# Kernel tuning notes

Measured on AMD Instinct MI355X. Metric: run time of the kernel, lower is better.

The kernel has to match this reference:

```python
import jax, jax.numpy as jnp
import numpy as np

H = 4  # num_heads

def setup_inputs() -> dict:
    key = jax.random.key(0)
    ks = jax.random.split(key, 9)
    B, S, D = 8, 2048, 256
    x = jax.random.normal(ks[0], (B, S, D), dtype=jnp.float32)
    scale = 1.0 / np.sqrt(D)
    Wq = jax.random.normal(ks[1], (D, D), dtype=jnp.float32) * scale
    bq = jnp.zeros((D,), dtype=jnp.float32)
    Wk = jax.random.normal(ks[2], (D, D), dtype=jnp.float32) * scale
    bk = jnp.zeros((D,), dtype=jnp.float32)
    Wv = jax.random.normal(ks[3], (D, D), dtype=jnp.float32) * scale
    bv = jnp.zeros((D,), dtype=jnp.float32)
    Wo = jax.random.normal(ks[4], (D, D), dtype=jnp.float32) * scale
    bo = jnp.zeros((D,), dtype=jnp.float32)
    return {"x": x, "Wq": Wq, "bq": bq, "Wk": Wk, "bk": bk,
            "Wv": Wv, "bv": bv, "Wo": Wo, "bo": bo}

def reference(x, Wq, bq, Wk, bk, Wv, bv, Wo, bo):
    B, S, D = x.shape
    hd = D // H
    inv_scale = 1.0 / jnp.sqrt(jnp.asarray(hd, x.dtype))
    # projections: torch Linear is x @ W.T + b; weights here stored as (D, D) used as x @ W + b
    def split_heads(t):
        return t.reshape(B, S, H, hd).transpose(0, 2, 1, 3)  # [B,H,S,hd]
    Q = split_heads(x @ Wq + bq)
    K = split_heads(x @ Wk + bk)
    V = split_heads(x @ Wv + bv)
    scores = jnp.einsum('bhqd,bhkd->bhqk', Q, K) * inv_scale  # [B,H,S,S]
    attn = jax.nn.softmax(scores, axis=-1)
    # dropout is identity in eval mode
    ctx = jnp.einsum('bhqk,bhkd->bhqd', attn, V)
    ctx = ctx.transpose(0, 2, 1, 3).reshape(B, S, D)
    return ctx @ Wo + bo
```

## Files before the change

kernel.cpp:

```cpp
#include <hip/hip_runtime.h>


typedef unsigned short u16;
typedef __bf16 bf16x8 __attribute__((ext_vector_type(8)));
typedef float  f32x4  __attribute__((ext_vector_type(4)));
typedef unsigned int u32x4 __attribute__((ext_vector_type(4)));
typedef unsigned int u32x2 __attribute__((ext_vector_type(2)));

#define LOG2E   1.4426950408889634f
#define ATTN_SC (0.125f * LOG2E)
#define PSTR    2097152
#define WPSTR   32768
#define WZSTR   65536

__device__ __forceinline__ u16 f2b(float f) {
  unsigned u = __builtin_bit_cast(unsigned, f);
  u += 0x7FFFu + ((u >> 16) & 1u);
  return (u16)(u >> 16);
}
__device__ __forceinline__ float b2f(u16 b) {
  return __builtin_bit_cast(float, (unsigned)b << 16);
}
__device__ __forceinline__ unsigned pack_trunc(float a, float b) {
  return (__builtin_bit_cast(unsigned, a) >> 16) | (__builtin_bit_cast(unsigned, b) & 0xFFFF0000u);
}
__device__ __forceinline__ unsigned pack_rne(float a, float b) {
  return (unsigned)f2b(a) | ((unsigned)f2b(b) << 16);
}
__device__ __forceinline__ f32x4 mfma16(bf16x8 a, bf16x8 b, f32x4 c) {
  return __builtin_amdgcn_mfma_f32_16x16x32_bf16(a, b, c, 0, 0, 0);
}
__device__ __forceinline__ void cp16(const u16* g, u16* l) {
  __builtin_amdgcn_global_load_lds((const __attribute__((address_space(1))) void*)g,
                                   (__attribute__((address_space(3))) void*)l, 16, 0, 0);
}

template <typename T>
__global__ __launch_bounds__(256) void prep(const T* __restrict__ x,
                                            const T* __restrict__ W0, const T* __restrict__ W1,
                                            const T* __restrict__ W2, const T* __restrict__ W3,
                                            const T* __restrict__ b0, const T* __restrict__ b1,
                                            const T* __restrict__ b2, const T* __restrict__ b3,
                                            u16* __restrict__ xp, u16* __restrict__ WTp,
                                            float* __restrict__ biasf) {
  int bid = blockIdx.x;
  if (bid < 4096) {
    int i0 = (bid * 256 + threadIdx.x) * 4;
    int row = i0 >> 8, col = i0 & 255;
    int p = col >> 7, pc = col & 127;
    u16* o = xp + (size_t)p * PSTR + (size_t)row * 128 + pc;
#pragma unroll
    for (int j = 0; j < 4; ++j) {
      if constexpr (sizeof(T) == 4) o[j] = f2b((float)x[i0 + j]);
      else                          o[j] = (u16)x[i0 + j];
    }
  } else {
    bid -= 4096;
    const int z = bid >> 8;
    const T* W = z == 0 ? W0 : z == 1 ? W1 : z == 2 ? W2 : W3;
    const T* b = z == 0 ? b0 : z == 1 ? b1 : z == 2 ? b2 : b3;
    int idx = (bid & 255) * 256 + threadIdx.x;
    int k = idx >> 8, n = idx & 255;
    u16 wb;
    if constexpr (sizeof(T) == 4) wb = f2b((float)W[k * 256 + n]);
    else                          wb = (u16)W[k * 256 + n];
    WTp[z * WZSTR + (k >> 7) * WPSTR + n * 128 + (k & 127)] = wb;
    if (idx < 256) {
      float bv;
      if constexpr (sizeof(T) == 4) bv = (float)b[idx];
      else                          bv = b2f((u16)b[idx]);
      biasf[z * 256 + idx] = bv;
    }
  }
}

__global__ __launch_bounds__(256, 2) void qkv_gemm(const u16* __restrict__ xp, const u16* __restrict__ WTp,
                                                   const float* __restrict__ biasf,
                                                   u16* __restrict__ Qw, u16* __restrict__ Kw,
                                                   u16* __restrict__ VTg) {
  __shared__ __align__(16) u16 Al[128 * 128];
  __shared__ __align__(16) u16 Bl[3][64 * 128];
  const int tid = threadIdx.x, w = tid >> 6, lane = tid & 63;
  const int l16 = lane & 15, quad = lane >> 4;
  const int n0 = blockIdx.y * 64, m0 = blockIdx.x * 128;
  f32x4 acc[3][2][4];
#pragma unroll
  for (int z = 0; z < 3; ++z)
#pragma unroll
    for (int mm = 0; mm < 2; ++mm)
#pragma unroll
      for (int nb = 0; nb < 4; ++nb) acc[z][mm][nb] = (f32x4){0.f, 0.f, 0.f, 0.f};

#pragma unroll
  for (int p = 0; p < 2; ++p) {
    __syncthreads();
    const u16* Ap = xp + (size_t)m0 * 128 + (size_t)p * PSTR;
#pragma unroll
    for (int i = 0; i < 8; ++i) {
      int slot = i * 256 + w * 64 + lane;
      int row = slot >> 4, pc = slot & 15, c = pc ^ (row & 15);
      cp16(Ap + (size_t)row * 128 + c * 8, Al + (i * 256 + w * 64) * 8);
    }
#pragma unroll
    for (int z = 0; z < 3; ++z) {
      const u16* Bp = WTp + z * WZSTR + n0 * 128 + p * WPSTR;
#pragma unroll
      for (int i = 0; i < 4; ++i) {
        int slot = i * 256 + w * 64 + lane;
        int row = slot >> 4, pc = slot & 15, c = pc ^ (row & 15);
        cp16(Bp + (size_t)row * 128 + c * 8, Bl[z] + (i * 256 + w * 64) * 8);
      }
    }
    __syncthreads();
#pragma unroll
    for (int kc = 0; kc < 4; ++kc) {
      bf16x8 a0 = *(const bf16x8*)&Al[(w * 32 + l16) * 128 + (((kc * 4 + quad) ^ l16)) * 8];
      bf16x8 a1 = *(const bf16x8*)&Al[(w * 32 + 16 + l16) * 128 + (((kc * 4 + quad) ^ l16)) * 8];
#pragma unroll
      for (int z = 0; z < 3; ++z)
#pragma unroll
        for (int nb = 0; nb < 4; ++nb) {
          bf16x8 b = *(const bf16x8*)&Bl[z][(nb * 16 + l16) * 128 + (((kc * 4 + quad) ^ l16)) * 8];
          acc[z][0][nb] = mfma16(a0, b, acc[z][0][nb]);
          acc[z][1][nb] = mfma16(a1, b, acc[z][1][nb]);
        }
    }
  }

  const int bb = m0 >> 11, s0 = m0 & 2047, h = blockIdx.y;
#pragma unroll
  for (int z = 0; z < 2; ++z) {
    u16* dst = (z == 0) ? Qw : Kw;
    const float sc = (z == 0) ? ATTN_SC : 1.0f;
    const float* bp = biasf + z * 256;
#pragma unroll
    for (int mm = 0; mm < 2; ++mm)
#pragma unroll
      for (int nb = 0; nb < 4; ++nb) {
        int d = nb * 16 + l16;
        float bv = bp[n0 + d];
#pragma unroll
        for (int r = 0; r < 4; ++r) {
          int s = s0 + w * 32 + mm * 16 + quad * 4 + r;
          dst[(((size_t)(bb * 4 + h) * 2048) + s) * 64 + d] = f2b((acc[z][mm][nb][r] + bv) * sc);
        }
      }
  }
  __syncthreads();
  {
    const float* bp = biasf + 2 * 256;
#pragma unroll
    for (int mm = 0; mm < 2; ++mm)
#pragma unroll
      for (int nb = 0; nb < 4; ++nb) {
        int d = nb * 16 + l16;
        float bv = bp[n0 + d];
        f32x4 v = acc[2][mm][nb];
        u32x2 dd = { pack_rne(v[0] + bv, v[1] + bv), pack_rne(v[2] + bv, v[3] + bv) };
        int cch = w * 4 + mm * 2 + (quad >> 1);
        *(u32x2*)&Bl[0][d * 128 + ((cch ^ (d & 15))) * 8 + (quad & 1) * 4] = dd;
      }
    __syncthreads();
#pragma unroll
    for (int i = 0; i < 4; ++i) {
      int slot = i * 256 + tid;
      int d = slot >> 4, pc = slot & 15;
      u32x4 vv = *(const u32x4*)&Bl[0][d * 128 + ((pc ^ (d & 15))) * 8];
      *(u32x4*)(VTg + (((size_t)(bb * 4 + h) * 64) + d) * 2048 + s0 + pc * 8) = vv;
    }
  }
}

template <bool OUT_BF16>
__global__ __launch_bounds__(256, 2) void out_gemm(const u16* __restrict__ ctxp, const u16* __restrict__ WTp,
                                                   const float* __restrict__ bo, void* __restrict__ outv) {
  __shared__ __align__(16) u16 Al[128 * 128];
  __shared__ __align__(16) u16 Bl[128 * 128];
  const int tid = threadIdx.x, w = tid >> 6, lane = tid & 63;
  const int l16 = lane & 15, quad = lane >> 4;
  const int n0 = blockIdx.y * 128, m0 = blockIdx.x * 128;
  f32x4 acc[2][8];
#pragma unroll
  for (int mm = 0; mm < 2; ++mm)
#pragma unroll
    for (int nb = 0; nb < 8; ++nb) acc[mm][nb] = (f32x4){0.f, 0.f, 0.f, 0.f};

#pragma unroll
  for (int p = 0; p < 2; ++p) {
    __syncthreads();
    const u16* Ap = ctxp + (size_t)m0 * 128 + (size_t)p * PSTR;
    const u16* Bp = WTp + 3 * WZSTR + n0 * 128 + p * WPSTR;
#pragma unroll
    for (int i = 0; i < 8; ++i) {
      int slot = i * 256 + w * 64 + lane;
      int row = slot >> 4, pc = slot & 15, c = pc ^ (row & 15);
      cp16(Ap + (size_t)row * 128 + c * 8, Al + (i * 256 + w * 64) * 8);
    }
#pragma unroll
    for (int i = 0; i < 8; ++i) {
      int slot = i * 256 + w * 64 + lane;
      int row = slot >> 4, pc = slot & 15, c = pc ^ (row & 15);
      cp16(Bp + (size_t)row * 128 + c * 8, Bl + (i * 256 + w * 64) * 8);
    }
    __syncthreads();
#pragma unroll
    for (int kc = 0; kc < 4; ++kc) {
      bf16x8 a0 = *(const bf16x8*)&Al[(w * 32 + l16) * 128 + (((kc * 4 + quad) ^ l16)) * 8];
      bf16x8 a1 = *(const bf16x8*)&Al[(w * 32 + 16 + l16) * 128 + (((kc * 4 + quad) ^ l16)) * 8];
#pragma unroll
      for (int nb = 0; nb < 8; ++nb) {
        bf16x8 b = *(const bf16x8*)&Bl[(nb * 16 + l16) * 128 + (((kc * 4 + quad) ^ l16)) * 8];
        acc[0][nb] = mfma16(a0, b, acc[0][nb]);
        acc[1][nb] = mfma16(a1, b, acc[1][nb]);
      }
    }
  }

#pragma unroll
  for (int mm = 0; mm < 2; ++mm)
#pragma unroll
    for (int nb = 0; nb < 8; ++nb) {
      int n = n0 + nb * 16 + l16;
      float bv = bo[n];
#pragma unroll
      for (int r = 0; r < 4; ++r) {
        size_t m = m0 + w * 32 + mm * 16 + quad * 4 + r;
        float v = acc[mm][nb][r] + bv;
        if constexpr (OUT_BF16) ((u16*)outv)[m * 256 + n] = f2b(v);
        else                    ((float*)outv)[m * 256 + n] = v;
      }
    }
}

__global__ __launch_bounds__(256, 2) void attn(const u16* __restrict__ Q, const u16* __restrict__ K,
                                               const u16* __restrict__ VT, u16* __restrict__ ctxp) {
  __shared__ __align__(16) u16 Kt[2][64 * 64];
  __shared__ __align__(16) u16 VTt[2][64 * 64];
  __shared__ __align__(16) u16 Pt[4][16 * 64];
  const int tid = threadIdx.x;
  const int w = tid >> 6, lane = tid & 63;
  const int l16 = lane & 15, quad = lane >> 4;
  const int bh = blockIdx.y, q0 = blockIdx.x * 128;
  const u16* Qp = Q + (size_t)bh * 2048 * 64;
  const u16* Kp = K + (size_t)bh * 2048 * 64;
  const u16* Vp = VT + (size_t)bh * 64 * 2048;
  u16* Ptw = Pt[w];

  bf16x8 qf[2][2];
#pragma unroll
  for (int h = 0; h < 2; ++h) {
    int qrow = q0 + w * 32 + h * 16 + l16;
    qf[h][0] = *(const bf16x8*)(Qp + (size_t)qrow * 64 + quad * 8);
    qf[h][1] = *(const bf16x8*)(Qp + (size_t)qrow * 64 + 32 + quad * 8);
  }

  f32x4 acc[2][4];
#pragma unroll
  for (int h = 0; h < 2; ++h)
#pragma unroll
    for (int nb = 0; nb < 4; ++nb) acc[h][nb] = (f32x4){0.f, 0.f, 0.f, 0.f};
  float dn0 = 0.f, dn1 = 0.f;

  const int sl0 = w * 64 + lane, sl1 = 256 + w * 64 + lane;
  const int r0 = sl0 >> 3, c0 = (sl0 & 7) ^ (r0 & 7);
  const int r1 = sl1 >> 3, c1 = (sl1 & 7) ^ (r1 & 7);
  const int pr0 = (r0 & 0x20) | ((r0 & 0x0C) << 1) | ((r0 & 0x10) >> 2) | (r0 & 3);
  const int pr1 = (r1 & 0x20) | ((r1 & 0x0C) << 1) | ((r1 & 0x10) >> 2) | (r1 & 3);

#define STAGE(kt_, buf_)                                                               \
  do {                                                                                 \
    cp16(Kp + (size_t)((kt_) * 64 + pr0) * 64 + c0 * 8, &Kt[buf_][(w * 64) * 8]);      \
    cp16(Kp + (size_t)((kt_) * 64 + pr1) * 64 + c1 * 8, &Kt[buf_][(256 + w * 64) * 8]);\
    cp16(Vp + (size_t)r0 * 2048 + (kt_) * 64 + c0 * 8, &VTt[buf_][(w * 64) * 8]);      \
    cp16(Vp + (size_t)r1 * 2048 + (kt_) * 64 + c1 * 8, &VTt[buf_][(256 + w * 64) * 8]);\
  } while (0)

  STAGE(0, 0);

  for (int kt = 0; kt < 32; ++kt) {
    const int buf = kt & 1;
    __builtin_amdgcn_s_waitcnt(0x0F70 );
    __asm__ __volatile__("" ::: "memory");
    __builtin_amdgcn_s_barrier();
    __asm__ __volatile__("" ::: "memory");
    if (kt < 31) STAGE(kt + 1, buf ^ 1);

    const u16* KtB = Kt[buf];
    const u16* VtB = VTt[buf];

    bf16x8 kfr[2][4];
#pragma unroll
    for (int kc = 0; kc < 2; ++kc)
#pragma unroll
      for (int nbK = 0; nbK < 4; ++nbK)
        kfr[kc][nbK] = *(const bf16x8*)&KtB[(nbK * 16 + l16) * 64 + (((kc * 4 + quad) ^ (l16 & 7))) * 8];
    bf16x8 vbr[2][4];
#pragma unroll
    for (int m = 0; m < 2; ++m)
#pragma unroll
      for (int nbD = 0; nbD < 4; ++nbD)
        vbr[m][nbD] = *(const bf16x8*)&VtB[(nbD * 16 + l16) * 64 + (((m * 4 + quad) ^ (l16 & 7))) * 8];

#pragma unroll
    for (int h = 0; h < 2; ++h) {
      f32x4 st[4];
#pragma unroll
      for (int nb = 0; nb < 4; ++nb) st[nb] = (f32x4){0.f, 0.f, 0.f, 0.f};
#pragma unroll
      for (int kc = 0; kc < 2; ++kc)
#pragma unroll
        for (int nbK = 0; nbK < 4; ++nbK)
          st[nbK] = mfma16(kfr[kc][nbK], qf[h][kc], st[nbK]);

      unsigned pw[8];
      float d = 0.f;
#pragma unroll
      for (int nbK = 0; nbK < 4; ++nbK) {
        float p0 = __builtin_amdgcn_exp2f(st[nbK][0]);
        float p1 = __builtin_amdgcn_exp2f(st[nbK][1]);
        float p2 = __builtin_amdgcn_exp2f(st[nbK][2]);
        float p3 = __builtin_amdgcn_exp2f(st[nbK][3]);
        d += (p0 + p1) + (p2 + p3);
        pw[nbK * 2]     = pack_trunc(p0, p1);
        pw[nbK * 2 + 1] = pack_trunc(p2, p3);
      }
      if (h == 0) dn0 += d; else dn1 += d;
      bf16x8 pb0 = __builtin_bit_cast(bf16x8, (u32x4){pw[0], pw[1], pw[2], pw[3]});
      bf16x8 pb1 = __builtin_bit_cast(bf16x8, (u32x4){pw[4], pw[5], pw[6], pw[7]});

#pragma unroll
      for (int nbD = 0; nbD < 4; ++nbD) acc[h][nbD] = mfma16(vbr[0][nbD], pb0, acc[h][nbD]);
#pragma unroll
      for (int nbD = 0; nbD < 4; ++nbD) acc[h][nbD] = mfma16(vbr[1][nbD], pb1, acc[h][nbD]);
    }
  }
#undef STAGE

  float linv0, linv1;
  { float d = dn0; d += __shfl_xor(d, 16); d += __shfl_xor(d, 32); linv0 = 1.0f / d; }
  { float d = dn1; d += __shfl_xor(d, 16); d += __shfl_xor(d, 32); linv1 = 1.0f / d; }

  const int bb = bh >> 2, hh = bh & 3;
  const int p = hh >> 1, pcol = (hh & 1) * 64;
#pragma unroll
  for (int h = 0; h < 2; ++h) {
    const float linv = h ? linv1 : linv0;
#pragma unroll
    for (int nbD = 0; nbD < 4; ++nbD) {
      f32x4 v = acc[h][nbD];
      u32x2 dd = { pack_rne(v[0] * linv, v[1] * linv), pack_rne(v[2] * linv, v[3] * linv) };
      int cch = nbD * 2 + (quad >> 1);
      *(u32x2*)&Ptw[l16 * 64 + ((cch ^ (l16 & 7))) * 8 + (quad & 1) * 4] = dd;
    }
    __asm__ __volatile__("" ::: "memory");
#pragma unroll
    for (int cc2 = 0; cc2 < 2; ++cc2) {
      int slot = cc2 * 64 + lane;
      int row = slot >> 3, pc = slot & 7;
      u32x4 vv = *(const u32x4*)&Ptw[row * 64 + ((pc ^ (row & 7))) * 8];
      size_t m = (size_t)bb * 2048 + q0 + w * 32 + h * 16 + row;
      *(u32x4*)&ctxp[(size_t)p * PSTR + m * 128 + pcol + pc * 8] = vv;
    }
    __asm__ __volatile__("" ::: "memory");
  }
}

extern "C" void kernel_launch(void* const* d_in, const int* in_sizes, int n_in,
                              void* d_out, int out_size, void* d_ws, size_t ws_size,
                              hipStream_t stream) {
  bool f32in = true;
  {
    void* basep = nullptr; size_t sz = 0;
    hipError_t e = hipMemGetAddressRange((hipDeviceptr_t*)&basep, &sz, (hipDeviceptr_t)d_in[0]);
    if (e == hipSuccess && sz > 0) f32in = sz >= (size_t)in_sizes[0] * 4;
    else f32in = false;
  }

  char* ws = (char*)d_ws;
  u16*   xp    = (u16*)(ws + 0);
  u16*   ctxp  = xp;
  u16*   WTp   = (u16*)(ws + 8388608);
  float* biasf = (float*)(ws + 8912896);
  u16*   Qw    = (u16*)(ws + 8916992);
  u16*   Kw    = (u16*)(ws + 17305600);
  u16*   VTg   = (u16*)(ws + 25694208);

  dim3 blk(256);
  if (f32in) {
    prep<float><<<5120, blk, 0, stream>>>(
        (const float*)d_in[0],
        (const float*)d_in[1], (const float*)d_in[3], (const float*)d_in[5], (const float*)d_in[7],
        (const float*)d_in[2], (const float*)d_in[4], (const float*)d_in[6], (const float*)d_in[8],
        xp, WTp, biasf);
  } else {
    prep<u16><<<5120, blk, 0, stream>>>(
        (const u16*)d_in[0],
        (const u16*)d_in[1], (const u16*)d_in[3], (const u16*)d_in[5], (const u16*)d_in[7],
        (const u16*)d_in[2], (const u16*)d_in[4], (const u16*)d_in[6], (const u16*)d_in[8],
        xp, WTp, biasf);
  }
  qkv_gemm<<<dim3(128, 4), blk, 0, stream>>>(xp, WTp, biasf, Qw, Kw, VTg);
  attn<<<dim3(16, 32), blk, 0, stream>>>(Qw, Kw, VTg, ctxp);
  if (f32in) out_gemm<false><<<dim3(128, 2), blk, 0, stream>>>(ctxp, WTp, biasf + 3 * 256, d_out);
  else       out_gemm<true ><<<dim3(128, 2), blk, 0, stream>>>(ctxp, WTp, biasf + 3 * 256, d_out);
}
```

Measured before the change: 146.2 us.

## Use two waves per attention block with 64 query rows each

The attention kernel now launches 128 threads per block instead of 256, and each wave handles 64 query rows instead of 32. Each K/V fragment loaded from shared memory is therefore reused across four 16-row query groups, which halves LDS read traffic per FLOP. The K and V fragment registers share one array so register pressure stays manageable. The cost is fewer waves per block and more accumulator registers per wave, which may lower occupancy and latency hiding, and each thread now issues twice as many global-to-LDS copies per stage.

```diff
diff --git a/kernel.cpp b/kernel.cpp
--- a/kernel.cpp
+++ b/kernel.cpp
@@ -232,11 +232,11 @@
     }
 }
 
-__global__ __launch_bounds__(256, 2) void attn(const u16* __restrict__ Q, const u16* __restrict__ K,
+__global__ __launch_bounds__(128, 1) void attn(const u16* __restrict__ Q, const u16* __restrict__ K,
                                                const u16* __restrict__ VT, u16* __restrict__ ctxp) {
   __shared__ __align__(16) u16 Kt[2][64 * 64];
   __shared__ __align__(16) u16 VTt[2][64 * 64];
-  __shared__ __align__(16) u16 Pt[4][16 * 64];
+  __shared__ __align__(16) u16 Pt[2][16 * 64];
   const int tid = threadIdx.x;
   const int w = tid >> 6, lane = tid & 63;
   const int l16 = lane & 15, quad = lane >> 4;
@@ -246,33 +246,40 @@
   const u16* Vp = VT + (size_t)bh * 64 * 2048;
   u16* Ptw = Pt[w];
 
-  bf16x8 qf[2][2];
-#pragma unroll
-  for (int h = 0; h < 2; ++h) {
-    int qrow = q0 + w * 32 + h * 16 + l16;
+  bf16x8 qf[4][2];
+#pragma unroll
+  for (int h = 0; h < 4; ++h) {
+    int qrow = q0 + w * 64 + h * 16 + l16;
     qf[h][0] = *(const bf16x8*)(Qp + (size_t)qrow * 64 + quad * 8);
     qf[h][1] = *(const bf16x8*)(Qp + (size_t)qrow * 64 + 32 + quad * 8);
   }
 
-  f32x4 acc[2][4];
-#pragma unroll
-  for (int h = 0; h < 2; ++h)
+  f32x4 acc[4][4];
+#pragma unroll
+  for (int h = 0; h < 4; ++h)
 #pragma unroll
     for (int nb = 0; nb < 4; ++nb) acc[h][nb] = (f32x4){0.f, 0.f, 0.f, 0.f};
-  float dn0 = 0.f, dn1 = 0.f;
-
-  const int sl0 = w * 64 + lane, sl1 = 256 + w * 64 + lane;
-  const int r0 = sl0 >> 3, c0 = (sl0 & 7) ^ (r0 & 7);
-  const int r1 = sl1 >> 3, c1 = (sl1 & 7) ^ (r1 & 7);
-  const int pr0 = (r0 & 0x20) | ((r0 & 0x0C) << 1) | ((r0 & 0x10) >> 2) | (r0 & 3);
-  const int pr1 = (r1 & 0x20) | ((r1 & 0x0C) << 1) | ((r1 & 0x10) >> 2) | (r1 & 3);
-
-#define STAGE(kt_, buf_)                                                               \
-  do {                                                                                 \
-    cp16(Kp + (size_t)((kt_) * 64 + pr0) * 64 + c0 * 8, &Kt[buf_][(w * 64) * 8]);      \
-    cp16(Kp + (size_t)((kt_) * 64 + pr1) * 64 + c1 * 8, &Kt[buf_][(256 + w * 64) * 8]);\
-    cp16(Vp + (size_t)r0 * 2048 + (kt_) * 64 + c0 * 8, &VTt[buf_][(w * 64) * 8]);      \
-    cp16(Vp + (size_t)r1 * 2048 + (kt_) * 64 + c1 * 8, &VTt[buf_][(256 + w * 64) * 8]);\
+  float dn[4] = {0.f, 0.f, 0.f, 0.f};
+
+  int rr[4], cc[4], pr[4];
+#pragma unroll
+  for (int i = 0; i < 4; ++i) {
+    int sl = i * 128 + w * 64 + lane;
+    rr[i] = sl >> 3;
+    cc[i] = (sl & 7) ^ (rr[i] & 7);
+    pr[i] = (rr[i] & 0x20) | ((rr[i] & 0x0C) << 1) | ((rr[i] & 0x10) >> 2) | (rr[i] & 3);
+  }
+
+#define STAGE(kt_, buf_)                                                                   \
+  do {                                                                                     \
+    _Pragma("unroll")                                                                      \
+    for (int i = 0; i < 4; ++i)                                                            \
+      cp16(Kp + (size_t)((kt_) * 64 + pr[i]) * 64 + cc[i] * 8,                             \
+           &Kt[buf_][(i * 128 + w * 64) * 8]);                                             \
+    _Pragma("unroll")                                                                      \
+    for (int i = 0; i < 4; ++i)                                                            \
+      cp16(Vp + (size_t)rr[i] * 2048 + (kt_) * 64 + cc[i] * 8,                             \
+           &VTt[buf_][(i * 128 + w * 64) * 8]);                                            \
   } while (0)
 
   STAGE(0, 0);
@@ -288,21 +295,16 @@
     const u16* KtB = Kt[buf];
     const u16* VtB = VTt[buf];
 
-    bf16x8 kfr[2][4];
+    bf16x8 fr[2][4];
 #pragma unroll
     for (int kc = 0; kc < 2; ++kc)
 #pragma unroll
       for (int nbK = 0; nbK < 4; ++nbK)
-        kfr[kc][nbK] = *(const bf16x8*)&KtB[(nbK * 16 + l16) * 64 + (((kc * 4 + quad) ^ (l16 & 7))) * 8];
-    bf16x8 vbr[2][4];
-#pragma unroll
-    for (int m = 0; m < 2; ++m)
-#pragma unroll
-      for (int nbD = 0; nbD < 4; ++nbD)
-        vbr[m][nbD] = *(const bf16x8*)&VtB[(nbD * 16 + l16) * 64 + (((m * 4 + quad) ^ (l16 & 7))) * 8];
-
-#pragma unroll
-    for (int h = 0; h < 2; ++h) {
+        fr[kc][nbK] = *(const bf16x8*)&KtB[(nbK * 16 + l16) * 64 + (((kc * 4 + quad) ^ (l16 & 7))) * 8];
+
+    bf16x8 pb[4][2];
+#pragma unroll
+    for (int h = 0; h < 4; ++h) {
       f32x4 st[4];
 #pragma unroll
       for (int nb = 0; nb < 4; ++nb) st[nb] = (f32x4){0.f, 0.f, 0.f, 0.f};
@@ -310,7 +312,7 @@
       for (int kc = 0; kc < 2; ++kc)
 #pragma unroll
         for (int nbK = 0; nbK < 4; ++nbK)
-          st[nbK] = mfma16(kfr[kc][nbK], qf[h][kc], st[nbK]);
+          st[nbK] = mfma16(fr[kc][nbK], qf[h][kc], st[nbK]);
 
       unsigned pw[8];
       float d = 0.f;
@@ -324,31 +326,45 @@
         pw[nbK * 2]     = pack_trunc(p0, p1);
         pw[nbK * 2 + 1] = pack_trunc(p2, p3);
       }
-      if (h == 0) dn0 += d; else dn1 += d;
-      bf16x8 pb0 = __builtin_bit_cast(bf16x8, (u32x4){pw[0], pw[1], pw[2], pw[3]});
-      bf16x8 pb1 = __builtin_bit_cast(bf16x8, (u32x4){pw[4], pw[5], pw[6], pw[7]});
-
-#pragma unroll
-      for (int nbD = 0; nbD < 4; ++nbD) acc[h][nbD] = mfma16(vbr[0][nbD], pb0, acc[h][nbD]);
-#pragma unroll
-      for (int nbD = 0; nbD < 4; ++nbD) acc[h][nbD] = mfma16(vbr[1][nbD], pb1, acc[h][nbD]);
+      dn[h] += d;
+      pb[h][0] = __builtin_bit_cast(bf16x8, (u32x4){pw[0], pw[1], pw[2], pw[3]});
+      pb[h][1] = __builtin_bit_cast(bf16x8, (u32x4){pw[4], pw[5], pw[6], pw[7]});
+    }
+
+#pragma unroll
+    for (int m = 0; m < 2; ++m)
+#pragma unroll
+      for (int nbD = 0; nbD < 4; ++nbD)
+        fr[m][nbD] = *(const bf16x8*)&VtB[(nbD * 16 + l16) * 64 + (((m * 4 + quad) ^ (l16 & 7))) * 8];
+
+#pragma unroll
+    for (int h = 0; h < 4; ++h) {
+#pragma unroll
+      for (int nbD = 0; nbD < 4; ++nbD) acc[h][nbD] = mfma16(fr[0][nbD], pb[h][0], acc[h][nbD]);
+#pragma unroll
+      for (int nbD = 0; nbD < 4; ++nbD) acc[h][nbD] = mfma16(fr[1][nbD], pb[h][1], acc[h][nbD]);
     }
   }
 #undef STAGE
 
-  float linv0, linv1;
-  { float d = dn0; d += __shfl_xor(d, 16); d += __shfl_xor(d, 32); linv0 = 1.0f / d; }
-  { float d = dn1; d += __shfl_xor(d, 16); d += __shfl_xor(d, 32); linv1 = 1.0f / d; }
+  float linv[4];
+#pragma unroll
+  for (int h = 0; h < 4; ++h) {
+    float d = dn[h];
+    d += __shfl_xor(d, 16);
+    d += __shfl_xor(d, 32);
+    linv[h] = 1.0f / d;
+  }
 
   const int bb = bh >> 2, hh = bh & 3;
   const int p = hh >> 1, pcol = (hh & 1) * 64;
 #pragma unroll
-  for (int h = 0; h < 2; ++h) {
-    const float linv = h ? linv1 : linv0;
+  for (int h = 0; h < 4; ++h) {
 #pragma unroll
     for (int nbD = 0; nbD < 4; ++nbD) {
       f32x4 v = acc[h][nbD];
-      u32x2 dd = { pack_rne(v[0] * linv, v[1] * linv), pack_rne(v[2] * linv, v[3] * linv) };
+      u32x2 dd = { pack_rne(v[0] * linv[h], v[1] * linv[h]),
+                   pack_rne(v[2] * linv[h], v[3] * linv[h]) };
       int cch = nbD * 2 + (quad >> 1);
       *(u32x2*)&Ptw[l16 * 64 + ((cch ^ (l16 & 7))) * 8 + (quad & 1) * 4] = dd;
     }
@@ -358,7 +374,7 @@
       int slot = cc2 * 64 + lane;
       int row = slot >> 3, pc = slot & 7;
       u32x4 vv = *(const u32x4*)&Ptw[row * 64 + ((pc ^ (row & 7))) * 8];
-      size_t m = (size_t)bb * 2048 + q0 + w * 32 + h * 16 + row;
+      size_t m = (size_t)bb * 2048 + q0 + w * 64 + h * 16 + row;
       *(u32x4*)&ctxp[(size_t)p * PSTR + m * 128 + pcol + pc * 8] = vv;
     }
     __asm__ __volatile__("" ::: "memory");
@@ -400,7 +416,7 @@
         xp, WTp, biasf);
   }
   qkv_gemm<<<dim3(128, 4), blk, 0, stream>>>(xp, WTp, biasf, Qw, Kw, VTg);
-  attn<<<dim3(16, 32), blk, 0, stream>>>(Qw, Kw, VTg, ctxp);
+  attn<<<dim3(16, 32), dim3(128), 0, stream>>>(Qw, Kw, VTg, ctxp);
   if (f32in) out_gemm<false><<<dim3(128, 2), blk, 0, stream>>>(ctxp, WTp, biasf + 3 * 256, d_out);
   else       out_gemm<true ><<<dim3(128, 2), blk, 0, stream>>>(ctxp, WTp, biasf + 3 * 256, d_out);
 }
```

New measurement: 164.3 us. +12.4%, slower.

## Triple-buffer K/V tiles in attention and raise wave priority around MFMAs

Applied to the files above, without the earlier changes.

The attention loop moves from double to triple buffering of the K and V^T LDS tiles, prefetching two tiles ahead. The waitcnt is relaxed so the oldest tile can complete while the next one is still in flight. s_setprio is raised around the MFMA blocks so waves issuing matrix ops get scheduling preference. LDS use grows from 32KB to 48KB for K/V, which may limit occupancy against the launch bound of two blocks per CU. Rotating the buffer pointers at run time may also add address arithmetic.

```diff
diff --git a/kernel.cpp b/kernel.cpp
--- a/kernel.cpp
+++ b/kernel.cpp
@@ -234,8 +234,8 @@
 
 __global__ __launch_bounds__(256, 2) void attn(const u16* __restrict__ Q, const u16* __restrict__ K,
                                                const u16* __restrict__ VT, u16* __restrict__ ctxp) {
-  __shared__ __align__(16) u16 Kt[2][64 * 64];
-  __shared__ __align__(16) u16 VTt[2][64 * 64];
+  __shared__ __align__(16) u16 Kt[3][64 * 64];
+  __shared__ __align__(16) u16 VTt[3][64 * 64];
   __shared__ __align__(16) u16 Pt[4][16 * 64];
   const int tid = threadIdx.x;
   const int w = tid >> 6, lane = tid & 63;
@@ -267,26 +267,29 @@
   const int pr0 = (r0 & 0x20) | ((r0 & 0x0C) << 1) | ((r0 & 0x10) >> 2) | (r0 & 3);
   const int pr1 = (r1 & 0x20) | ((r1 & 0x0C) << 1) | ((r1 & 0x10) >> 2) | (r1 & 3);
 
-#define STAGE(kt_, buf_)                                                               \
-  do {                                                                                 \
-    cp16(Kp + (size_t)((kt_) * 64 + pr0) * 64 + c0 * 8, &Kt[buf_][(w * 64) * 8]);      \
-    cp16(Kp + (size_t)((kt_) * 64 + pr1) * 64 + c1 * 8, &Kt[buf_][(256 + w * 64) * 8]);\
-    cp16(Vp + (size_t)r0 * 2048 + (kt_) * 64 + c0 * 8, &VTt[buf_][(w * 64) * 8]);      \
-    cp16(Vp + (size_t)r1 * 2048 + (kt_) * 64 + c1 * 8, &VTt[buf_][(256 + w * 64) * 8]);\
+#define STAGE(kt_, KB_, VB_)                                                        \
+  do {                                                                              \
+    cp16(Kp + (size_t)((kt_) * 64 + pr0) * 64 + c0 * 8, (KB_) + (w * 64) * 8);      \
+    cp16(Kp + (size_t)((kt_) * 64 + pr1) * 64 + c1 * 8, (KB_) + (256 + w * 64) * 8);\
+    cp16(Vp + (size_t)r0 * 2048 + (kt_) * 64 + c0 * 8, (VB_) + (w * 64) * 8);       \
+    cp16(Vp + (size_t)r1 * 2048 + (kt_) * 64 + c1 * 8, (VB_) + (256 + w * 64) * 8); \
   } while (0)
 
-  STAGE(0, 0);
+  u16 *Ka = Kt[0], *Kb = Kt[1], *Kc = Kt[2];
+  u16 *Va = VTt[0], *Vb = VTt[1], *Vc = VTt[2];
+  STAGE(0, Ka, Va);
+  STAGE(1, Kb, Vb);
 
   for (int kt = 0; kt < 32; ++kt) {
-    const int buf = kt & 1;
-    __builtin_amdgcn_s_waitcnt(0x0F70 );
+    if (kt == 31) __builtin_amdgcn_s_waitcnt(0x0F70);
+    else          __builtin_amdgcn_s_waitcnt(0x0F74);
     __asm__ __volatile__("" ::: "memory");
     __builtin_amdgcn_s_barrier();
     __asm__ __volatile__("" ::: "memory");
-    if (kt < 31) STAGE(kt + 1, buf ^ 1);
-
-    const u16* KtB = Kt[buf];
-    const u16* VtB = VTt[buf];
+    if (kt < 30) STAGE(kt + 2, Kc, Vc);
+
+    const u16* KtB = Ka;
+    const u16* VtB = Va;
 
     bf16x8 kfr[2][4];
 #pragma unroll
@@ -306,11 +309,13 @@
       f32x4 st[4];
 #pragma unroll
       for (int nb = 0; nb < 4; ++nb) st[nb] = (f32x4){0.f, 0.f, 0.f, 0.f};
+      __builtin_amdgcn_s_setprio(1);
 #pragma unroll
       for (int kc = 0; kc < 2; ++kc)
 #pragma unroll
         for (int nbK = 0; nbK < 4; ++nbK)
           st[nbK] = mfma16(kfr[kc][nbK], qf[h][kc], st[nbK]);
+      __builtin_amdgcn_s_setprio(0);
 
       unsigned pw[8];
       float d = 0.f;
@@ -328,11 +333,17 @@
       bf16x8 pb0 = __builtin_bit_cast(bf16x8, (u32x4){pw[0], pw[1], pw[2], pw[3]});
       bf16x8 pb1 = __builtin_bit_cast(bf16x8, (u32x4){pw[4], pw[5], pw[6], pw[7]});
 
+      __builtin_amdgcn_s_setprio(1);
 #pragma unroll
       for (int nbD = 0; nbD < 4; ++nbD) acc[h][nbD] = mfma16(vbr[0][nbD], pb0, acc[h][nbD]);
 #pragma unroll
       for (int nbD = 0; nbD < 4; ++nbD) acc[h][nbD] = mfma16(vbr[1][nbD], pb1, acc[h][nbD]);
-    }
+      __builtin_amdgcn_s_setprio(0);
+    }
+
+    u16* t;
+    t = Ka; Ka = Kb; Kb = Kc; Kc = t;
+    t = Va; Va = Vb; Vb = Vc; Vc = t;
   }
 #undef STAGE
 
```

Measured after the change: 143.5 us. No clear change (-1.9%).
